# Kernel optimization log

Hardware: AMD Instinct MI355X
Metric: run time of the kernel (lower is better)

The kernel has to match this reference:

```python
import jax, jax.numpy as jnp
import numpy as np


def _dependence(X):
    # X: [N, D]. dom[i, j] = True iff X[i, d] > X[j, d] for all d.
    # Diagonal is automatically False (X[i] > X[i] is all False), matching the
    # original's explicit i != j exclusion.
    dom = jnp.all(X[:, None, :] > X[None, :, :], axis=-1)  # [N, N] bool
    n = X.shape[0]
    Z = dom.sum(axis=1).astype(X.dtype) / (n - 1)  # [N]
    return Z


def setup_inputs() -> dict:
    key = jax.random.key(0)
    k1, k2 = jax.random.split(key)
    N, D = 8192, 8
    X = jax.random.normal(k1, (N, D), dtype=jnp.float32)
    X_hat = jax.random.normal(k2, (N, D), dtype=jnp.float32)
    return {"X": X, "X_hat": X_hat}


def reference(X, X_hat):
    Z = jnp.sort(_dependence(X))
    Zhat = jnp.sort(_dependence(X_hat))
    return jnp.sum(jnp.abs(Z - Zhat)) / Z.shape[0]
```

## Files before the change

### kernel.cpp

```cpp
#include <hip/hip_runtime.h>

constexpr int N = 8192;
constexpr int BLK = 256;
constexpr int IPT = 4;
constexpr int ITILE = BLK * IPT;
constexpr int JTILE = 256;
constexpr int JCH = N / JTILE;

__global__ __launch_bounds__(BLK) void dom_count_kernel(
    const float* __restrict__ X, const float* __restrict__ Xh,
    int* __restrict__ counts) {
  const float* M = (blockIdx.z == 0) ? X : Xh;
  int* cnt_out = counts + blockIdx.z * N;

  __shared__ float4 tile[JTILE * 2];

  const int tid = threadIdx.x;
  const int ibase = blockIdx.x * ITILE + tid;

  const int j0 = blockIdx.y * JTILE;
  const float4* src = reinterpret_cast<const float4*>(M + (size_t)j0 * 8);
  for (int k = tid; k < JTILE * 2; k += BLK) tile[k] = src[k];

  float4 r0[IPT], r1[IPT];
#pragma unroll
  for (int p = 0; p < IPT; ++p) {
    const float4* Mi = reinterpret_cast<const float4*>(M + (size_t)(ibase + p * BLK) * 8);
    r0[p] = Mi[0];
    r1[p] = Mi[1];
  }
  __syncthreads();

  int cnt[IPT] = {};
#pragma unroll 2
  for (int j = 0; j < JTILE; ++j) {
    const float4 a = tile[2 * j];
    const float4 b = tile[2 * j + 1];
#pragma unroll
    for (int p = 0; p < IPT; ++p) {
      const float m0 = fminf(fminf(r0[p].x - a.x, r0[p].y - a.y),
                             fminf(r0[p].z - a.z, r0[p].w - a.w));
      const float m1 = fminf(fminf(r1[p].x - b.x, r1[p].y - b.y),
                             fminf(r1[p].z - b.z, r1[p].w - b.w));
      cnt[p] += (fminf(m0, m1) > 0.0f) ? 1 : 0;
    }
  }
#pragma unroll
  for (int p = 0; p < IPT; ++p) atomicAdd(&cnt_out[ibase + p * BLK], cnt[p]);
}

__global__ __launch_bounds__(1024) void finalize_kernel(
    const int* __restrict__ counts, float* __restrict__ out) {
  __shared__ int hist[N];
  __shared__ int wsum[16];
  __shared__ int wexc[16];
  __shared__ int wabs[16];

  const int tid = threadIdx.x;
  const int lane = tid & 63;
  const int wid = tid >> 6;

  for (int k = tid; k < N; k += 1024) hist[k] = 0;
  __syncthreads();

  for (int k = tid; k < N; k += 1024) {
    atomicAdd(&hist[counts[k]], 1);
    atomicAdd(&hist[counts[N + k]], -1);
  }
  __syncthreads();

  int local[8];
  int s = 0;
#pragma unroll
  for (int q = 0; q < 8; ++q) {
    local[q] = hist[tid * 8 + q];
    s += local[q];
  }

  int incl = s;
#pragma unroll
  for (int off = 1; off < 64; off <<= 1) {
    const int v = __shfl_up(incl, off);
    if (lane >= off) incl += v;
  }
  if (lane == 63) wsum[wid] = incl;
  __syncthreads();

  if (tid == 0) {
    int acc = 0;
#pragma unroll
    for (int w = 0; w < 16; ++w) { wexc[w] = acc; acc += wsum[w]; }
  }
  __syncthreads();

  int run = wexc[wid] + (incl - s);
  int acc = 0;
#pragma unroll
  for (int q = 0; q < 8; ++q) {
    run += local[q];
    acc += (run < 0) ? -run : run;
  }

#pragma unroll
  for (int off = 32; off > 0; off >>= 1) acc += __shfl_down(acc, off);
  if (lane == 0) wabs[wid] = acc;
  __syncthreads();

  if (tid == 0) {
    int total = 0;
#pragma unroll
    for (int w = 0; w < 16; ++w) total += wabs[w];
    out[0] = (float)((double)total / ((double)(N - 1) * (double)N));
  }
}

extern "C" void kernel_launch(void* const* d_in, const int* in_sizes, int n_in,
                              void* d_out, int out_size, void* d_ws, size_t ws_size,
                              hipStream_t stream) {
  const float* X = (const float*)d_in[0];
  const float* Xh = (const float*)d_in[1];
  float* out = (float*)d_out;
  int* counts = (int*)d_ws;

  hipMemsetAsync(counts, 0, 2 * N * sizeof(int), stream);

  dim3 grid(N / ITILE, JCH, 2);
  dom_count_kernel<<<grid, BLK, 0, stream>>>(X, Xh, counts);
  finalize_kernel<<<1, 1024, 0, stream>>>(counts, out);
}
```

Baseline: 110.9 us.

## Use v_min3 in dominance test and parallelize histogram across blocks

```diff
diff --git a/kernel.cpp b/kernel.cpp
--- a/kernel.cpp
+++ b/kernel.cpp
@@ -6,6 +6,17 @@
 constexpr int ITILE = BLK * IPT;
 constexpr int JTILE = 256;
 constexpr int JCH = N / JTILE;
+
+__device__ __forceinline__ float min3f(float a, float b, float c) {
+  float r;
+  asm("v_min3_f32 %0, %1, %2, %3" : "=v"(r) : "v"(a), "v"(b), "v"(c));
+  return r;
+}
+__device__ __forceinline__ float min2f(float a, float b) {
+  float r;
+  asm("v_min_f32 %0, %1, %2" : "=v"(r) : "v"(a), "v"(b));
+  return r;
+}
 
 __global__ __launch_bounds__(BLK) void dom_count_kernel(
     const float* __restrict__ X, const float* __restrict__ Xh,
@@ -38,20 +49,39 @@
     const float4 b = tile[2 * j + 1];
 #pragma unroll
     for (int p = 0; p < IPT; ++p) {
-      const float m0 = fminf(fminf(r0[p].x - a.x, r0[p].y - a.y),
-                             fminf(r0[p].z - a.z, r0[p].w - a.w));
-      const float m1 = fminf(fminf(r1[p].x - b.x, r1[p].y - b.y),
-                             fminf(r1[p].z - b.z, r1[p].w - b.w));
-      cnt[p] += (fminf(m0, m1) > 0.0f) ? 1 : 0;
+      const float t0 = min3f(r0[p].x - a.x, r0[p].y - a.y, r0[p].z - a.z);
+      const float t1 = min3f(r0[p].w - a.w, r1[p].x - b.x, r1[p].y - b.y);
+      const float t2 = min2f(r1[p].z - b.z, r1[p].w - b.w);
+      cnt[p] += (min3f(t0, t1, t2) > 0.0f) ? 1 : 0;
     }
   }
 #pragma unroll
   for (int p = 0; p < IPT; ++p) atomicAdd(&cnt_out[ibase + p * BLK], cnt[p]);
 }
 
+constexpr int HB = 16;
+__global__ __launch_bounds__(1024) void hist_partial_kernel(
+    const int* __restrict__ counts, int* __restrict__ ghist) {
+  __shared__ int lhist[N];
+  const int tid = threadIdx.x;
+  for (int q = tid; q < N; q += 1024) lhist[q] = 0;
+  __syncthreads();
+
+  const int k = blockIdx.x * (2 * N / HB) + tid;
+  const int v = counts[k];
+  atomicAdd(&lhist[v], (k < N) ? 1 : -1);
+  __syncthreads();
+
+#pragma unroll
+  for (int q = 0; q < N / 1024; ++q) {
+    const int bin = tid * (N / 1024) + q;
+    const int h = lhist[bin];
+    if (h != 0) atomicAdd(&ghist[bin], h);
+  }
+}
+
 __global__ __launch_bounds__(1024) void finalize_kernel(
-    const int* __restrict__ counts, float* __restrict__ out) {
-  __shared__ int hist[N];
+    const int* __restrict__ ghist, float* __restrict__ out) {
   __shared__ int wsum[16];
   __shared__ int wexc[16];
   __shared__ int wabs[16];
@@ -60,20 +90,11 @@
   const int lane = tid & 63;
   const int wid = tid >> 6;
 
-  for (int k = tid; k < N; k += 1024) hist[k] = 0;
-  __syncthreads();
-
-  for (int k = tid; k < N; k += 1024) {
-    atomicAdd(&hist[counts[k]], 1);
-    atomicAdd(&hist[counts[N + k]], -1);
-  }
-  __syncthreads();
-
   int local[8];
   int s = 0;
 #pragma unroll
   for (int q = 0; q < 8; ++q) {
-    local[q] = hist[tid * 8 + q];
+    local[q] = ghist[tid * 8 + q];
     s += local[q];
   }
 
@@ -121,10 +142,12 @@
   const float* Xh = (const float*)d_in[1];
   float* out = (float*)d_out;
   int* counts = (int*)d_ws;
+  int* ghist = counts + 2 * N;
 
-  hipMemsetAsync(counts, 0, 2 * N * sizeof(int), stream);
+  hipMemsetAsync(counts, 0, (2 * N + N) * sizeof(int), stream);
 
   dim3 grid(N / ITILE, JCH, 2);
   dom_count_kernel<<<grid, BLK, 0, stream>>>(X, Xh, counts);
-  finalize_kernel<<<1, 1024, 0, stream>>>(counts, out);
+  hist_partial_kernel<<<HB, 1024, 0, stream>>>(counts, ghist);
+  finalize_kernel<<<1, 1024, 0, stream>>>(ghist, out);
 }
```

After: 104.7 us. 1.06x faster.
